# Optimization experiments

Measured on AMD Instinct MI355X. Metric: run time of the kernel, lower is better.

## Reference

```python
import jax, jax.numpy as jnp
import numpy as np

FEAT_DIM = 512
N_NODES = 65536


def setup_inputs() -> dict:
    key = jax.random.key(0)
    kq, kk, kv, ko = jax.random.split(key, 4)
    # scale inputs so exp(omega @ x) stays well within fp32 range
    Q = jax.random.normal(kq, (N_NODES, FEAT_DIM), dtype=jnp.float32) * 0.1
    K = jax.random.normal(kk, (N_NODES, FEAT_DIM), dtype=jnp.float32) * 0.1
    V = jax.random.normal(kv, (N_NODES, FEAT_DIM), dtype=jnp.float32)
    # omega = Gram-Schmidt (QR) orthogonalization of a Gaussian matrix, as in make_rand_feats
    G = jax.random.normal(ko, (FEAT_DIM, FEAT_DIM), dtype=jnp.float32)
    omega, _ = jnp.linalg.qr(G)
    return {"Q": Q, "K": K, "V": V, "omega": omega}


def _make_phi(x, omega):
    # omega_x[k, i] = sum_j omega[i, j] * x[k, j]  ->  x @ omega^T, shape [n, m]
    omega_x = x @ omega.T
    m = omega_x.shape[1]
    # h = exp(-||x||^2 / 2), shape [n, 1]
    h = jnp.exp(-0.5 * jnp.sum(x * x, axis=-1, keepdims=True))
    return (h / jnp.sqrt(jnp.float32(m))) * jnp.exp(omega_x)


def reference(Q, K, V, omega):
    Q_hat = _make_phi(Q, omega)  # [n, m]
    K_hat = _make_phi(K, omega)  # [n, m]
    # k_ones = K_hat^T @ 1  (column sums), shape [m]
    k_ones = jnp.sum(K_hat, axis=0)
    # d_diag = Q_hat @ k_ones, shape [n]; division replaces the n x n diag matmul
    d_diag = Q_hat @ k_ones
    kv = K_hat.T @ V            # [m, d_v]
    qkv = Q_hat @ kv            # [n, d_v]
    return qkv / d_diag[:, None]
```

## Files before the change

kernel.cpp:

```cpp
#include <hip/hip_runtime.h>
#include <hip/hip_bf16.h>


typedef __bf16 bf16x8 __attribute__((ext_vector_type(8)));
typedef float f32x4 __attribute__((ext_vector_type(4)));
typedef unsigned short ushort_t;
typedef ushort_t u16x8 __attribute__((ext_vector_type(8)));
typedef ushort_t u16x4 __attribute__((ext_vector_type(4)));

#define N_NODES 65536
#define FEAT 512

__device__ __forceinline__ ushort_t f2b(float f) {
  unsigned u = __builtin_bit_cast(unsigned, f);
  unsigned r = (u + 0x7fffu + ((u >> 16) & 1u)) >> 16;
  return (ushort_t)r;
}
__device__ __forceinline__ float b2f(ushort_t u) {
  return __builtin_bit_cast(float, ((unsigned)u) << 16);
}

__device__ __forceinline__ void load16(const ushort_t* g, ushort_t* l) {
  __builtin_amdgcn_global_load_lds((const __attribute__((address_space(1))) void*)g,
                                   (__attribute__((address_space(3))) void*)l, 16, 0, 0);
}

__global__ __launch_bounds__(256) void k_zero(float* __restrict__ p, int n) {
  int i = blockIdx.x * 256 + threadIdx.x;
  if (i < n) p[i] = 0.f;
}

__device__ __forceinline__ void gemm_tile(const ushort_t* A, const ushort_t* B,
                                          long lda, long ldb, int ksteps,
                                          ushort_t* lA, ushort_t* lB, f32x4 acc[4][4]) {
  const int tid = threadIdx.x;
  const int lane = tid & 63;
  const int wid = tid >> 6;
  const int wr = wid >> 1, wc = wid & 1;
  const int lrow = lane & 15;
  const int lk8 = (lane >> 4) * 8;

  for (int kt = 0; kt < ksteps; ++kt) {
    const ushort_t* Ak = A + (size_t)kt * 64;
    const ushort_t* Bk = B + (size_t)kt * 64;
#pragma unroll
    for (int r = 0; r < 4; ++r) {
      int slot = tid + r * 256;
      int row = slot >> 3;
      int col = (slot & 7) * 8;
      load16(Ak + (size_t)row * lda + col, lA + slot * 8);
      load16(Bk + (size_t)row * ldb + col, lB + slot * 8);
    }
    __syncthreads();
#pragma unroll
    for (int ks = 0; ks < 2; ++ks) {
      bf16x8 af[4], bb[4];
#pragma unroll
      for (int mi = 0; mi < 4; ++mi)
        af[mi] = *(const bf16x8*)(lA + ((wr * 64 + mi * 16 + lrow) * 64 + ks * 32 + lk8));
#pragma unroll
      for (int ni = 0; ni < 4; ++ni)
        bb[ni] = *(const bf16x8*)(lB + ((wc * 64 + ni * 16 + lrow) * 64 + ks * 32 + lk8));
#pragma unroll
      for (int mi = 0; mi < 4; ++mi)
#pragma unroll
        for (int ni = 0; ni < 4; ++ni)
          acc[mi][ni] = __builtin_amdgcn_mfma_f32_16x16x32_bf16(af[mi], bb[ni], acc[mi][ni], 0, 0, 0);
    }
    __syncthreads();
  }
}

__global__ __launch_bounds__(256) void k_prep_omega(const float* __restrict__ om,
                                                    ushort_t* __restrict__ Ob) {
  int i = blockIdx.x * 256 + threadIdx.x;
  float4 v = ((const float4*)om)[i];
  u16x4 o = {f2b(v.x), f2b(v.y), f2b(v.z), f2b(v.w)};
  ((u16x4*)Ob)[i] = o;
}

__global__ __launch_bounds__(256) void k_vt(const float* __restrict__ V,
                                            ushort_t* __restrict__ VT) {
  __shared__ ushort_t t[64][72];
  int r0 = blockIdx.x * 64;
  int c0 = blockIdx.y * 64;
#pragma unroll
  for (int it = 0; it < 4; ++it) {
    int slot = threadIdx.x + it * 256;
    int r = slot >> 4;
    int c4 = slot & 15;
    float4 v = *(const float4*)(V + (size_t)(r0 + r) * FEAT + c0 + c4 * 4);
    u16x4 p = {f2b(v.x), f2b(v.y), f2b(v.z), f2b(v.w)};
    *(u16x4*)&t[r][c4 * 4] = p;
  }
  __syncthreads();
#pragma unroll
  for (int it = 0; it < 2; ++it) {
    int slot = threadIdx.x + it * 256;
    int dr = slot >> 3;
    int n8 = slot & 7;
    u16x8 o;
#pragma unroll
    for (int j = 0; j < 8; ++j) o[j] = t[n8 * 8 + j][dr];
    *(u16x8*)(VT + (size_t)(c0 + dr) * N_NODES + r0 + n8 * 8) = o;
  }
}

template <int TRANSK>
__global__ __launch_bounds__(256) void k_phi_fused(const float* __restrict__ X,
                                                   const ushort_t* __restrict__ Ob,
                                                   const float* __restrict__ k1,
                                                   float* __restrict__ k1w,
                                                   float* __restrict__ dd,
                                                   ushort_t* __restrict__ Out) {
  __shared__ ushort_t lA[128 * 64], lB[128 * 64];
  __shared__ float cvbuf[128];
  f32x4 acc[4][4];
#pragma unroll
  for (int i = 0; i < 4; ++i)
#pragma unroll
    for (int j = 0; j < 4; ++j) acc[i][j] = (f32x4){0.f, 0.f, 0.f, 0.f};

  const int tid = threadIdx.x;
  const int lane = tid & 63;
  const int wid = tid >> 6;
  const int wr = wid >> 1, wc = wid & 1;
  const int lrow = lane & 15;
  const int lk8 = (lane >> 4) * 8;
  const int m0 = blockIdx.y * 128, n0 = blockIdx.x * 128;
  const float* Ax = X + (size_t)m0 * FEAT;
  const ushort_t* Bo = Ob + (size_t)n0 * FEAT;
  const int arow = tid >> 3;
  const int acol = (tid & 7) * 8;
  float nacc[4] = {0.f, 0.f, 0.f, 0.f};

  for (int kt = 0; kt < 8; ++kt) {
#pragma unroll
    for (int r = 0; r < 4; ++r) {
      int slot = tid + r * 256;
      int row = slot >> 3;
      int col = (slot & 7) * 8;
      load16(Bo + (size_t)row * FEAT + kt * 64 + col, lB + slot * 8);
    }
#pragma unroll
    for (int r = 0; r < 4; ++r) {
      int row = arow + r * 32;
      const float* src = Ax + (size_t)row * FEAT + kt * 64 + acol;
      float4 a0 = *(const float4*)src;
      float4 a1 = *(const float4*)(src + 4);
      nacc[r] += a0.x * a0.x + a0.y * a0.y + a0.z * a0.z + a0.w * a0.w
               + a1.x * a1.x + a1.y * a1.y + a1.z * a1.z + a1.w * a1.w;
      u16x8 p = {f2b(a0.x), f2b(a0.y), f2b(a0.z), f2b(a0.w),
                 f2b(a1.x), f2b(a1.y), f2b(a1.z), f2b(a1.w)};
      *(u16x8*)(lA + (size_t)(tid + r * 256) * 8) = p;
    }
    __syncthreads();
#pragma unroll
    for (int ks = 0; ks < 2; ++ks) {
      bf16x8 af[4], bb[4];
#pragma unroll
      for (int mi = 0; mi < 4; ++mi)
        af[mi] = *(const bf16x8*)(lA + ((wr * 64 + mi * 16 + lrow) * 64 + ks * 32 + lk8));
#pragma unroll
      for (int ni = 0; ni < 4; ++ni)
        bb[ni] = *(const bf16x8*)(lB + ((wc * 64 + ni * 16 + lrow) * 64 + ks * 32 + lk8));
#pragma unroll
      for (int mi = 0; mi < 4; ++mi)
#pragma unroll
        for (int ni = 0; ni < 4; ++ni)
          acc[mi][ni] = __builtin_amdgcn_mfma_f32_16x16x32_bf16(af[mi], bb[ni], acc[mi][ni], 0, 0, 0);
    }
    __syncthreads();
  }

#pragma unroll
  for (int r = 0; r < 4; ++r) {
    float s = nacc[r];
    s += __shfl_xor(s, 1, 64);
    s += __shfl_xor(s, 2, 64);
    s += __shfl_xor(s, 4, 64);
    if ((lane & 7) == 0) cvbuf[arow + r * 32] = -0.5f * s - 3.11916231f;
  }
  __syncthreads();

  const int cbase = n0 + wc * 64 + lrow;
  const int lrbase = wr * 64 + ((lane >> 4) << 2);
  float colp[4] = {0.f, 0.f, 0.f, 0.f};
  float k1v[4];
  if (!TRANSK) {
#pragma unroll
    for (int ni = 0; ni < 4; ++ni) k1v[ni] = k1[cbase + ni * 16];
  }
#pragma unroll
  for (int mi = 0; mi < 4; ++mi) {
    int lr0 = lrbase + mi * 16;
    float cv[4];
#pragma unroll
    for (int j = 0; j < 4; ++j) cv[j] = cvbuf[lr0 + j];
    if (TRANSK) {
#pragma unroll
      for (int ni = 0; ni < 4; ++ni) {
        int col = cbase + ni * 16;
        u16x4 pk;
#pragma unroll
        for (int j = 0; j < 4; ++j) {
          float e = __expf(acc[mi][ni][j] + cv[j]);
          pk[j] = f2b(e);
          colp[ni] += e;
        }
        *(u16x4*)(Out + (size_t)col * N_NODES + m0 + lr0) = pk;
      }
    } else {
#pragma unroll
      for (int j = 0; j < 4; ++j) {
        float t = 0.f;
#pragma unroll
        for (int ni = 0; ni < 4; ++ni) {
          float e = __expf(acc[mi][ni][j] + cv[j]);
          Out[(size_t)(m0 + lr0 + j) * FEAT + cbase + ni * 16] = f2b(e);
          t += e * k1v[ni];
        }
        t += __shfl_xor(t, 1, 64);
        t += __shfl_xor(t, 2, 64);
        t += __shfl_xor(t, 4, 64);
        t += __shfl_xor(t, 8, 64);
        if (lrow == 0) atomicAdd(&dd[m0 + lr0 + j], t);
      }
    }
  }
  if (TRANSK) {
#pragma unroll
    for (int ni = 0; ni < 4; ++ni) {
      float t = colp[ni];
      t += __shfl_xor(t, 16, 64);
      t += __shfl_xor(t, 32, 64);
      if (lane < 16) atomicAdd(&k1w[n0 + wc * 64 + lane + ni * 16], t);
    }
  }
}

__global__ __launch_bounds__(256) void k_kv(const ushort_t* __restrict__ KT,
                                            const ushort_t* __restrict__ VT,
                                            float* __restrict__ P) {
  __shared__ ushort_t lA[128 * 64], lB[128 * 64];
  f32x4 acc[4][4];
#pragma unroll
  for (int i = 0; i < 4; ++i)
#pragma unroll
    for (int j = 0; j < 4; ++j) acc[i][j] = (f32x4){0.f, 0.f, 0.f, 0.f};
  const int m0 = blockIdx.y * 128, n0 = blockIdx.x * 128, z = blockIdx.z;
  gemm_tile(KT + (size_t)m0 * N_NODES + z * 2048,
            VT + (size_t)n0 * N_NODES + z * 2048, N_NODES, N_NODES, 32, lA, lB, acc);
  float* Pz = P + (size_t)z * (FEAT * FEAT);
  const int lane = threadIdx.x & 63, wid = threadIdx.x >> 6;
  const int wr = wid >> 1, wc = wid & 1;
  const int cbase = n0 + wc * 64 + (lane & 15);
  const int rbase = m0 + wr * 64 + ((lane >> 4) << 2);
#pragma unroll
  for (int mi = 0; mi < 4; ++mi)
#pragma unroll
    for (int ni = 0; ni < 4; ++ni)
#pragma unroll
      for (int j = 0; j < 4; ++j)
        Pz[(size_t)(rbase + mi * 16 + j) * FEAT + cbase + ni * 16] = acc[mi][ni][j];
}

__global__ __launch_bounds__(256) void k_redkv(const float* __restrict__ P,
                                               ushort_t* __restrict__ kvT) {
  int t = blockIdx.x * 256 + threadIdx.x;
  int m = t >> 7;
  int d4 = t & 127;
  float4 s = {0.f, 0.f, 0.f, 0.f};
  for (int z = 0; z < 32; ++z) {
    float4 v = *(const float4*)(P + (size_t)z * (FEAT * FEAT) + (size_t)m * FEAT + d4 * 4);
    s.x += v.x; s.y += v.y; s.z += v.z; s.w += v.w;
  }
  kvT[(size_t)(d4 * 4 + 0) * FEAT + m] = f2b(s.x);
  kvT[(size_t)(d4 * 4 + 1) * FEAT + m] = f2b(s.y);
  kvT[(size_t)(d4 * 4 + 2) * FEAT + m] = f2b(s.z);
  kvT[(size_t)(d4 * 4 + 3) * FEAT + m] = f2b(s.w);
}

__global__ __launch_bounds__(256) void k_final(const ushort_t* __restrict__ Qh,
                                               const ushort_t* __restrict__ kvT,
                                               const float* __restrict__ dd,
                                               float* __restrict__ out) {
  __shared__ ushort_t lA[128 * 64], lB[128 * 64];
  f32x4 acc[4][4];
#pragma unroll
  for (int i = 0; i < 4; ++i)
#pragma unroll
    for (int j = 0; j < 4; ++j) acc[i][j] = (f32x4){0.f, 0.f, 0.f, 0.f};
  const int m0 = blockIdx.y * 128, n0 = blockIdx.x * 128;
  gemm_tile(Qh + (size_t)m0 * FEAT, kvT + (size_t)n0 * FEAT, FEAT, FEAT, 8, lA, lB, acc);
  const int lane = threadIdx.x & 63, wid = threadIdx.x >> 6;
  const int wr = wid >> 1, wc = wid & 1;
  const int cbase = n0 + wc * 64 + (lane & 15);
  const int rbase = m0 + wr * 64 + ((lane >> 4) << 2);
#pragma unroll
  for (int mi = 0; mi < 4; ++mi) {
    int r0 = rbase + mi * 16;
    float inv[4];
#pragma unroll
    for (int j = 0; j < 4; ++j) inv[j] = 1.0f / dd[r0 + j];
#pragma unroll
    for (int ni = 0; ni < 4; ++ni) {
      int col = cbase + ni * 16;
#pragma unroll
      for (int j = 0; j < 4; ++j)
        out[(size_t)(r0 + j) * FEAT + col] = acc[mi][ni][j] * inv[j];
    }
  }
}

extern "C" void kernel_launch(void* const* d_in, const int* in_sizes, int n_in,
                              void* d_out, int out_size, void* d_ws, size_t ws_size,
                              hipStream_t stream) {
  const float* Q = (const float*)d_in[0];
  const float* K = (const float*)d_in[1];
  const float* V = (const float*)d_in[2];
  const float* omega = (const float*)d_in[3];
  float* out = (float*)d_out;

  char* ws = (char*)d_ws;
  ushort_t* B1  = (ushort_t*)(ws);
  ushort_t* B2  = (ushort_t*)(ws + 67108864);
  ushort_t* Ob  = (ushort_t*)(ws + 134217728);
  ushort_t* kvT = (ushort_t*)(ws + 134742016);
  float*    k1  = (float*)(ws + 135266304);
  float*    dd  = (float*)(ws + 135268352);
  float*    P   = (float*)d_out;

  k_zero<<<(512 + 65536 + 255) / 256, 256, 0, stream>>>(k1, 512 + 65536);
  k_prep_omega<<<256, 256, 0, stream>>>(omega, Ob);
  k_phi_fused<1><<<dim3(4, 512), 256, 0, stream>>>(K, Ob, k1, k1, dd, B2);
  k_vt<<<dim3(N_NODES / 64, 8), 256, 0, stream>>>(V, B1);
  k_kv<<<dim3(4, 4, 32), 256, 0, stream>>>(B2, B1, P);
  k_phi_fused<0><<<dim3(4, 512), 256, 0, stream>>>(Q, Ob, k1, k1, dd, B2);
  k_redkv<<<256, 256, 0, stream>>>(P, kvT);
  k_final<<<dim3(4, 512), 256, 0, stream>>>(B2, kvT, dd, out);
}
```

Baseline: 689.0 us.

## Swizzle LDS tiles, prefetch fp32 A rows, and merge init kernels

Applies an XOR swizzle to the LDS layout of the 64-wide bf16 tiles in the shared GEMM helper and in the fused phi kernel, so the MFMA fragment reads avoid bank conflicts. The fused phi kernel now register-prefetches the next K-step of fp32 input rows while the MFMAs run, overlapping global latency with compute at the cost of extra registers. The zeroing and omega-conversion kernels are merged into one launch to save a kernel launch. The swizzle has to match on the write and read sides in every kernel that uses these tiles; the code not shown must be consistent with it.

```diff
diff --git a/kernel.cpp b/kernel.cpp
--- a/kernel.cpp
+++ b/kernel.cpp
@@ -25,9 +25,20 @@
                                    (__attribute__((address_space(3))) void*)l, 16, 0, 0);
 }
 
-__global__ __launch_bounds__(256) void k_zero(float* __restrict__ p, int n) {
-  int i = blockIdx.x * 256 + threadIdx.x;
-  if (i < n) p[i] = 0.f;
+
+__global__ __launch_bounds__(256) void k_init(const float* __restrict__ om,
+                                              ushort_t* __restrict__ Ob,
+                                              float* __restrict__ zp, int zn) {
+  int b = blockIdx.x;
+  if (b < 256) {
+    int i = b * 256 + threadIdx.x;
+    float4 v = ((const float4*)om)[i];
+    u16x4 o = {f2b(v.x), f2b(v.y), f2b(v.z), f2b(v.w)};
+    ((u16x4*)Ob)[i] = o;
+  } else {
+    int i = (b - 256) * 256 + threadIdx.x;
+    if (i < zn) zp[i] = 0.f;
+  }
 }
 
 __device__ __forceinline__ void gemm_tile(const ushort_t* A, const ushort_t* B,
@@ -38,7 +49,7 @@
   const int wid = tid >> 6;
   const int wr = wid >> 1, wc = wid & 1;
   const int lrow = lane & 15;
-  const int lk8 = (lane >> 4) * 8;
+  const int swz = lrow & 7;
 
   for (int kt = 0; kt < ksteps; ++kt) {
     const ushort_t* Ak = A + (size_t)kt * 64;
@@ -47,20 +58,21 @@
     for (int r = 0; r < 4; ++r) {
       int slot = tid + r * 256;
       int row = slot >> 3;
-      int col = (slot & 7) * 8;
-      load16(Ak + (size_t)row * lda + col, lA + slot * 8);
-      load16(Bk + (size_t)row * ldb + col, lB + slot * 8);
+      int gsrc = (slot & 7) ^ (row & 7);
+      load16(Ak + (size_t)row * lda + gsrc * 8, lA + slot * 8);
+      load16(Bk + (size_t)row * ldb + gsrc * 8, lB + slot * 8);
     }
     __syncthreads();
 #pragma unroll
     for (int ks = 0; ks < 2; ++ks) {
+      const int gsw = ((ks * 4 + (lane >> 4)) ^ swz) * 8;
       bf16x8 af[4], bb[4];
 #pragma unroll
       for (int mi = 0; mi < 4; ++mi)
-        af[mi] = *(const bf16x8*)(lA + ((wr * 64 + mi * 16 + lrow) * 64 + ks * 32 + lk8));
+        af[mi] = *(const bf16x8*)(lA + ((wr * 64 + mi * 16 + lrow) * 64 + gsw));
 #pragma unroll
       for (int ni = 0; ni < 4; ++ni)
-        bb[ni] = *(const bf16x8*)(lB + ((wc * 64 + ni * 16 + lrow) * 64 + ks * 32 + lk8));
+        bb[ni] = *(const bf16x8*)(lB + ((wc * 64 + ni * 16 + lrow) * 64 + gsw));
 #pragma unroll
       for (int mi = 0; mi < 4; ++mi)
 #pragma unroll
@@ -69,14 +81,6 @@
     }
     __syncthreads();
   }
-}
-
-__global__ __launch_bounds__(256) void k_prep_omega(const float* __restrict__ om,
-                                                    ushort_t* __restrict__ Ob) {
-  int i = blockIdx.x * 256 + threadIdx.x;
-  float4 v = ((const float4*)om)[i];
-  u16x4 o = {f2b(v.x), f2b(v.y), f2b(v.z), f2b(v.w)};
-  ((u16x4*)Ob)[i] = o;
 }
 
 __global__ __launch_bounds__(256) void k_vt(const float* __restrict__ V,
@@ -126,7 +130,7 @@
   const int wid = tid >> 6;
   const int wr = wid >> 1, wc = wid & 1;
   const int lrow = lane & 15;
-  const int lk8 = (lane >> 4) * 8;
+  const int swz = lrow & 7;
   const int m0 = blockIdx.y * 128, n0 = blockIdx.x * 128;
   const float* Ax = X + (size_t)m0 * FEAT;
   const ushort_t* Bo = Ob + (size_t)n0 * FEAT;
@@ -134,36 +138,52 @@
   const int acol = (tid & 7) * 8;
   float nacc[4] = {0.f, 0.f, 0.f, 0.f};
 
+  float4 pa0[4], pa1[4];
+#pragma unroll
+  for (int r = 0; r < 4; ++r) {
+    const float* src = Ax + (size_t)(arow + r * 32) * FEAT + acol;
+    pa0[r] = *(const float4*)src;
+    pa1[r] = *(const float4*)(src + 4);
+  }
+
   for (int kt = 0; kt < 8; ++kt) {
 #pragma unroll
     for (int r = 0; r < 4; ++r) {
       int slot = tid + r * 256;
       int row = slot >> 3;
-      int col = (slot & 7) * 8;
-      load16(Bo + (size_t)row * FEAT + kt * 64 + col, lB + slot * 8);
+      int gsrc = (slot & 7) ^ (row & 7);
+      load16(Bo + (size_t)row * FEAT + kt * 64 + gsrc * 8, lB + slot * 8);
     }
 #pragma unroll
     for (int r = 0; r < 4; ++r) {
       int row = arow + r * 32;
-      const float* src = Ax + (size_t)row * FEAT + kt * 64 + acol;
-      float4 a0 = *(const float4*)src;
-      float4 a1 = *(const float4*)(src + 4);
+      float4 a0 = pa0[r], a1 = pa1[r];
       nacc[r] += a0.x * a0.x + a0.y * a0.y + a0.z * a0.z + a0.w * a0.w
                + a1.x * a1.x + a1.y * a1.y + a1.z * a1.z + a1.w * a1.w;
       u16x8 p = {f2b(a0.x), f2b(a0.y), f2b(a0.z), f2b(a0.w),
                  f2b(a1.x), f2b(a1.y), f2b(a1.z), f2b(a1.w)};
-      *(u16x8*)(lA + (size_t)(tid + r * 256) * 8) = p;
+      int gl = (tid & 7) ^ (row & 7);
+      *(u16x8*)(lA + (size_t)row * 64 + gl * 8) = p;
     }
     __syncthreads();
+    if (kt < 7) {
+#pragma unroll
+      for (int r = 0; r < 4; ++r) {
+        const float* src = Ax + (size_t)(arow + r * 32) * FEAT + (kt + 1) * 64 + acol;
+        pa0[r] = *(const float4*)src;
+        pa1[r] = *(const float4*)(src + 4);
+      }
+    }
 #pragma unroll
     for (int ks = 0; ks < 2; ++ks) {
+      const int gsw = ((ks * 4 + (lane >> 4)) ^ swz) * 8;
       bf16x8 af[4], bb[4];
 #pragma unroll
       for (int mi = 0; mi < 4; ++mi)
-        af[mi] = *(const bf16x8*)(lA + ((wr * 64 + mi * 16 + lrow) * 64 + ks * 32 + lk8));
+        af[mi] = *(const bf16x8*)(lA + ((wr * 64 + mi * 16 + lrow) * 64 + gsw));
 #pragma unroll
       for (int ni = 0; ni < 4; ++ni)
-        bb[ni] = *(const bf16x8*)(lB + ((wc * 64 + ni * 16 + lrow) * 64 + ks * 32 + lk8));
+        bb[ni] = *(const bf16x8*)(lB + ((wc * 64 + ni * 16 + lrow) * 64 + gsw));
 #pragma unroll
       for (int mi = 0; mi < 4; ++mi)
 #pragma unroll
@@ -331,8 +351,7 @@
   float*    dd  = (float*)(ws + 135268352);
   float*    P   = (float*)d_out;
 
-  k_zero<<<(512 + 65536 + 255) / 256, 256, 0, stream>>>(k1, 512 + 65536);
-  k_prep_omega<<<256, 256, 0, stream>>>(omega, Ob);
+  k_init<<<256 + 258, 256, 0, stream>>>(omega, Ob, k1, 512 + 65536);
   k_phi_fused<1><<<dim3(4, 512), 256, 0, stream>>>(K, Ob, k1, k1, dd, B2);
   k_vt<<<dim3(N_NODES / 64, 8), 256, 0, stream>>>(V, B1);
   k_kv<<<dim3(4, 4, 32), 256, 0, stream>>>(B2, B1, P);
```

Result: faster. 665.9 us (-3.3%).
